# Kernel tuning notes

Measured on AMD Instinct MI355X. Metric: run time of the kernel, lower is better.

Reference implementation:

```python
import jax, jax.numpy as jnp
import numpy as np

STRIDE = 1
PAD = 1
DIL = 1


def setup_inputs() -> dict:
    key = jax.random.key(0)
    k1, k2, k3 = jax.random.split(key, 3)
    N, Cin, H, W = 8, 128, 96, 96
    Cout, Kh, Kw = 256, 3, 3
    inp = jax.random.normal(k1, (N, Cin, H, W), dtype=jnp.float32)
    # offset channels: 2*Kh*Kw per offset group (1 group), layout (dy, dx) pairs
    offset = jax.random.normal(k2, (N, 2 * Kh * Kw, H, W), dtype=jnp.float32)
    weight = jax.random.normal(k3, (Cout, Cin, Kh, Kw), dtype=jnp.float32) * 0.05
    return {"input": inp, "offset": offset, "weight": weight}


def _deform_conv(inp, offset, weight):
    N, Cin, H, W = inp.shape
    Cout, _, Kh, Kw = weight.shape
    K = Kh * Kw
    Ho = (H + 2 * PAD - DIL * (Kh - 1) - 1) // STRIDE + 1
    Wo = (W + 2 * PAD - DIL * (Kw - 1) - 1) // STRIDE + 1

    # base sampling grid (before learned offsets)
    hs = jnp.arange(Ho, dtype=inp.dtype) * STRIDE - PAD          # [Ho]
    ws = jnp.arange(Wo, dtype=inp.dtype) * STRIDE - PAD          # [Wo]
    ky, kx = jnp.meshgrid(jnp.arange(Kh, dtype=inp.dtype) * DIL,
                          jnp.arange(Kw, dtype=inp.dtype) * DIL,
                          indexing="ij")
    ky = ky.reshape(K)
    kx = kx.reshape(K)

    off = offset.reshape(N, K, 2, Ho, Wo)                        # pairs (dy, dx)
    py = hs[None, None, :, None] + ky[None, :, None, None] + off[:, :, 0]  # [N,K,Ho,Wo]
    px = ws[None, None, None, :] + kx[None, :, None, None] + off[:, :, 1]  # [N,K,Ho,Wo]

    y0 = jnp.floor(py)
    x0 = jnp.floor(px)
    ly = py - y0   # fractional parts
    lx = px - x0
    y0i = y0.astype(jnp.int32)
    x0i = x0.astype(jnp.int32)

    img = inp.transpose(0, 2, 3, 1)                              # [N,H,W,Cin]
    bidx = jnp.arange(N)[:, None, None, None]

    def gather(yi, xi):
        valid = (yi >= 0) & (yi < H) & (xi >= 0) & (xi < W)
        yc = jnp.clip(yi, 0, H - 1)
        xc = jnp.clip(xi, 0, W - 1)
        v = img[bidx, yc, xc]                                    # [N,K,Ho,Wo,Cin]
        return v * valid[..., None].astype(img.dtype)

    v00 = gather(y0i, x0i)
    v01 = gather(y0i, x0i + 1)
    v10 = gather(y0i + 1, x0i)
    v11 = gather(y0i + 1, x0i + 1)

    wy, wx = ly[..., None], lx[..., None]
    samp = (v00 * (1 - wy) * (1 - wx) + v01 * (1 - wy) * wx
            + v10 * wy * (1 - wx) + v11 * wy * wx)               # [N,K,Ho,Wo,Cin]

    w2 = weight.reshape(Cout, Cin, K)
    return jnp.einsum("nkhwc,ock->nohw", samp, w2)               # [N,Cout,Ho,Wo]


def reference(input, offset, weight):
    return _deform_conv(input, offset, weight)
```

## Files before the change

### kernel.cpp

```cpp
#include <hip/hip_runtime.h>
#include <hip/hip_bf16.h>
#include <hip/hip_fp16.h>

#define NN   8
#define CIN  128
#define HH   96
#define WW   96
#define COUT 256
#define KK   9
#define HO   96
#define WO   96
#define PTOT (NN*HO*WO)
#define BM   64
#define KTOT (CIN*KK)
#define KSTEPS (KTOT/32)

typedef _Float16 f16x8 __attribute__((ext_vector_type(8)));
typedef float f32x4  __attribute__((ext_vector_type(4)));

__device__ __forceinline__ __half2 u2h2(unsigned u) {
    union { unsigned u; __half2 h; } c; c.u = u; return c.h;
}
__device__ __forceinline__ unsigned h22u(__half2 h) {
    union { unsigned u; __half2 h; } c; c.h = h; return c.u;
}
__device__ __forceinline__ unsigned pack_h2(float a, float b) {
    auto v = __builtin_amdgcn_cvt_pkrtz(a, b);
    union { decltype(v) h; unsigned u; } c; c.h = v; return c.u;
}

__global__ __launch_bounds__(256) void to_nhwc_f16(const float* __restrict__ in,
                                                   unsigned short* __restrict__ outp) {
    __shared__ float tile[CIN * 97];
    const int ny = blockIdx.x;
    const int n = ny / HH, y = ny - n * HH;
    const float* src = in + (size_t)n * CIN * HH * WW + (size_t)y * WW;
    for (int i = threadIdx.x; i < CIN * WW; i += 256) {
        int c = i / WW, x = i - c * WW;
        tile[c * 97 + x] = src[(size_t)c * HH * WW + x];
    }
    __syncthreads();
    unsigned* dst = (unsigned*)(outp + (size_t)ny * WW * CIN);
    for (int i = threadIdx.x; i < (WW * CIN) / 2; i += 256) {
        int c2 = (i & 63) * 2;
        int x  = i >> 6;
        dst[x * (CIN / 2) + (c2 >> 1)] = pack_h2(tile[c2 * 97 + x], tile[(c2 + 1) * 97 + x]);
    }
}

__global__ __launch_bounds__(256) void w_pack(const float* __restrict__ w,
                                              unsigned short* __restrict__ wp) {
    int idx = blockIdx.x * 256 + threadIdx.x;
    if (idx >= KSTEPS * 16 * 64 * 8) return;
    int j  = idx & 7;
    int l  = (idx >> 3) & 63;
    int cb = (idx >> 9) & 15;
    int ks = idx >> 13;
    int co  = cb * 16 + (l & 15);
    int kg  = ks * 32 + ((l >> 4) * 8) + j;
    int tap = kg >> 7;
    int cin = kg & 127;
    _Float16 h = (_Float16)w[((size_t)co * CIN + cin) * KK + tap];
    wp[idx] = *(unsigned short*)&h;
}

#define GEOM_BYTES 6912
#define LDS_BYTES  39680
#define BUF0 6912
#define BUF1 23296

__global__ __launch_bounds__(512, 6) void deform_mfma(
    const unsigned short* __restrict__ imgB,
    const float*          __restrict__ off,
    const unsigned short* __restrict__ wPack,
    float*                __restrict__ out)
{
    __shared__ __align__(16) char smem[LDS_BYTES];
    unsigned* gOff = (unsigned*)smem;
    unsigned* gW0  = (unsigned*)(smem + 2304);
    unsigned* gW1  = (unsigned*)(smem + 4608);

    const int t    = threadIdx.x;
    const int lane = t & 63;
    const int wv   = t >> 6;

    const int bid  = ((blockIdx.x & 7) * ((PTOT / BM) >> 3)) + (blockIdx.x >> 3);

    const int p0   = bid * BM;
    const int nb   = p0 / (HO * WO);
    const int p0rem = p0 - nb * (HO * WO);

    for (int i = t; i < KK * BM; i += 512) {
        int tap = i >> 6, m = i & 63;
        int plin = p0rem + m;
        int ho = plin / WO, wo = plin - ho * WO;
        int kh = tap / 3, kw = tap - kh * 3;
        const float* ob = off + ((size_t)nb * 2 * KK + 2 * tap) * (HO * WO) + plin;
        float py = (float)(ho - 1 + kh) + ob[0];
        float px = (float)(wo - 1 + kw) + ob[HO * WO];
        float y0f = floorf(py), x0f = floorf(px);
        float ly = py - y0f, lx = px - x0f;
        int y0 = (int)y0f, x0 = (int)x0f;

        bool vy0 = (unsigned)y0 < (unsigned)HH;
        bool vy1 = (unsigned)(y0 + 1) < (unsigned)HH;
        bool vx0 = (unsigned)x0 < (unsigned)WW;
        bool vx1 = (unsigned)(x0 + 1) < (unsigned)WW;
        int yc0 = min(max(y0, 0), HH - 1);
        int yc1 = min(max(y0 + 1, 0), HH - 1);
        int xc0 = min(max(x0, 0), WW - 1);
        int xc1 = min(max(x0 + 1, 0), WW - 1);

        float w11 = ly * lx;
        float w10 = ly - w11;
        float w01 = lx - w11;
        float w00 = 1.f - ly - lx + w11;
        w00 = (vy0 && vx0) ? w00 : 0.f;
        w01 = (vy0 && vx1) ? w01 : 0.f;
        w10 = (vy1 && vx0) ? w10 : 0.f;
        w11 = (vy1 && vx1) ? w11 : 0.f;

        unsigned byte00 = (unsigned)(yc0 * WW + xc0) * (CIN * 2);
        unsigned xs = (xc1 != xc0) ? 1u : 0u;
        unsigned ys = (yc1 != yc0) ? 1u : 0u;
        gOff[i] = byte00 | (xs << 22) | (ys << 23);
        gW0[i]  = pack_h2(w00, w01);
        gW1[i]  = pack_h2(w10, w11);
    }

    f32x4 acc[4][2];
#pragma unroll
    for (int mf = 0; mf < 4; ++mf)
#pragma unroll
        for (int nf = 0; nf < 2; ++nf) acc[mf][nf] = (f32x4)0.f;

    const char* imgN = (const char*)(imgB + (size_t)nb * (HH * WW) * CIN);

    auto gather = [&](int tap, char* bufw) {
#pragma unroll
        for (int it = 0; it < 2; ++it) {
            int item  = t + it * 512;
            int pos   = item >> 4;
            int chunk = item & 15;
            int gi    = tap * 64 + pos;

            unsigned ofl  = gOff[gi];
            unsigned w0pk = gW0[gi];
            unsigned w1pk = gW1[gi];

            unsigned a00 = (ofl & 0x3fffffu) + (unsigned)(chunk * 16);
            unsigned dx  = (ofl >> 14) & 0x100u;
            unsigned dy  = ((ofl >> 23) & 1u) * 24576u;

            uint4 r00 = *(const uint4*)(imgN + a00);
            uint4 r01 = *(const uint4*)(imgN + a00 + dx);
            uint4 r10 = *(const uint4*)(imgN + a00 + dy);
            uint4 r11 = *(const uint4*)(imgN + a00 + dy + dx);

            unsigned u00 = w0pk & 0xffffu;      u00 |= u00 << 16;
            unsigned u01 = w0pk >> 16;          u01 |= u01 << 16;
            unsigned u10 = w1pk & 0xffffu;      u10 |= u10 << 16;
            unsigned u11 = w1pk >> 16;          u11 |= u11 << 16;
            __half2 w00s = u2h2(u00), w01s = u2h2(u01);
            __half2 w10s = u2h2(u10), w11s = u2h2(u11);

            unsigned pk[4];
            __half2 s;
            s = __hmul2(u2h2(r11.x), w11s);
            s = __hfma2(u2h2(r10.x), w10s, s);
            s = __hfma2(u2h2(r01.x), w01s, s);
            s = __hfma2(u2h2(r00.x), w00s, s);
            pk[0] = h22u(s);
            s = __hmul2(u2h2(r11.y), w11s);
            s = __hfma2(u2h2(r10.y), w10s, s);
            s = __hfma2(u2h2(r01.y), w01s, s);
            s = __hfma2(u2h2(r00.y), w00s, s);
            pk[1] = h22u(s);
            s = __hmul2(u2h2(r11.z), w11s);
            s = __hfma2(u2h2(r10.z), w10s, s);
            s = __hfma2(u2h2(r01.z), w01s, s);
            s = __hfma2(u2h2(r00.z), w00s, s);
            pk[2] = h22u(s);
            s = __hmul2(u2h2(r11.w), w11s);
            s = __hfma2(u2h2(r10.w), w10s, s);
            s = __hfma2(u2h2(r01.w), w01s, s);
            s = __hfma2(u2h2(r00.w), w00s, s);
            pk[3] = h22u(s);

            int byte = pos * 256 + chunk * 16;
            byte ^= (pos & 15) << 4;
            *(uint4*)(bufw + byte) = make_uint4(pk[0], pk[1], pk[2], pk[3]);
        }
    };

    __syncthreads();
    gather(0, smem + BUF0);

    for (int tap = 0; tap < KK; ++tap) {
        __syncthreads();
        const char* bufr = smem + ((tap & 1) ? BUF1 : BUF0);

#pragma unroll
        for (int cs = 0; cs < 4; ++cs) {
            int ks = tap * 4 + cs;
            f16x8 a[4], b[2];
#pragma unroll
            for (int mf = 0; mf < 4; ++mf) {
                int row  = mf * 16 + (lane & 15);
                int byte = row * 256 + cs * 64 + ((lane >> 4) * 16);
                byte ^= (row & 15) << 4;
                a[mf] = *(const f16x8*)(bufr + byte);
            }
#pragma unroll
            for (int nf = 0; nf < 2; ++nf) {
                int tile = ks * 16 + (wv * 2 + nf);
                b[nf] = *(const f16x8*)(wPack + (size_t)tile * 512 + lane * 8);
            }
            __builtin_amdgcn_s_setprio(1);
#pragma unroll
            for (int mf = 0; mf < 4; ++mf)
#pragma unroll
                for (int nf = 0; nf < 2; ++nf)
                    acc[mf][nf] = __builtin_amdgcn_mfma_f32_16x16x32_f16(
                        a[mf], b[nf], acc[mf][nf], 0, 0, 0);
            __builtin_amdgcn_s_setprio(0);
        }

        if (tap + 1 < KK) gather(tap + 1, smem + ((tap & 1) ? BUF0 : BUF1));
    }

    __syncthreads();
    float* cT = (float*)smem + wv * (32 * 20);
    const int colbase = lane & 15;
    const int rowq    = lane >> 4;
    const int co2     = lane & 31;
    const int half    = lane >> 5;
    float* outbase = out + ((size_t)nb * COUT + wv * 32 + co2) * (HO * WO) + p0rem;
#pragma unroll
    for (int mf = 0; mf < 4; ++mf) {
#pragma unroll
        for (int nf = 0; nf < 2; ++nf) {
            int co = nf * 16 + colbase;
            *(f32x4*)&cT[co * 20 + rowq * 4] = acc[mf][nf];
        }
        asm volatile("s_waitcnt lgkmcnt(0)" ::: "memory");
        __builtin_amdgcn_sched_barrier(0);
        f32x4 v0 = *(f32x4*)&cT[co2 * 20 + half * 8];
        f32x4 v1 = *(f32x4*)&cT[co2 * 20 + half * 8 + 4];
        *(float4*)(outbase + mf * 16 + half * 8)     = *(float4*)&v0;
        *(float4*)(outbase + mf * 16 + half * 8 + 4) = *(float4*)&v1;
    }
}

__global__ __launch_bounds__(256) void deform_fallback(const float* __restrict__ img,
                                                       const float* __restrict__ off,
                                                       const float* __restrict__ wgt,
                                                       float* __restrict__ out) {
    __shared__ float samp[8][CIN];
    const int tid = threadIdx.x;
    const int p0  = blockIdx.x * 8;
    const int n   = p0 / (HO * WO);
    const int rem = p0 % (HO * WO);
    const int ho  = rem / WO;
    const int wo0 = rem % WO;
    float acc[8];
#pragma unroll
    for (int t = 0; t < 8; ++t) acc[t] = 0.f;
    for (int k = 0; k < KK; ++k) {
        __syncthreads();
        const int kh = k / 3, kw = k % 3;
#pragma unroll
        for (int it = 0; it < 4; ++it) {
            int idx = tid + it * 256;
            int t   = idx >> 7;
            int c   = idx & (CIN - 1);
            int wo  = wo0 + t;
            float dy = off[(((size_t)n * 2 * KK + 2 * k) * HO + ho) * WO + wo];
            float dx = off[(((size_t)n * 2 * KK + 2 * k + 1) * HO + ho) * WO + wo];
            float py = (float)(ho - 1 + kh) + dy;
            float px = (float)(wo - 1 + kw) + dx;
            float y0f = floorf(py), x0f = floorf(px);
            float ly = py - y0f, lx = px - x0f;
            int y0 = (int)y0f, x0 = (int)x0f;
            float v00 = 0.f, v01 = 0.f, v10 = 0.f, v11 = 0.f;
            const float* base = img + ((size_t)n * CIN + c) * HH * WW;
            if ((unsigned)y0 < (unsigned)HH) {
                const float* row = base + (size_t)y0 * WW;
                if ((unsigned)x0 < (unsigned)WW)       v00 = row[x0];
                if ((unsigned)(x0 + 1) < (unsigned)WW) v01 = row[x0 + 1];
            }
            if ((unsigned)(y0 + 1) < (unsigned)HH) {
                const float* row = base + (size_t)(y0 + 1) * WW;
                if ((unsigned)x0 < (unsigned)WW)       v10 = row[x0];
                if ((unsigned)(x0 + 1) < (unsigned)WW) v11 = row[x0 + 1];
            }
            float top = v00 + lx * (v01 - v00);
            float bot = v10 + lx * (v11 - v10);
            samp[t][c] = top + ly * (bot - top);
        }
        __syncthreads();
        const float* wk = wgt + (size_t)tid * CIN * KK + k;
        for (int c = 0; c < CIN; c += 4) {
            float w0 = wk[(c + 0) * KK], w1 = wk[(c + 1) * KK];
            float w2 = wk[(c + 2) * KK], w3 = wk[(c + 3) * KK];
#pragma unroll
            for (int t = 0; t < 8; ++t) {
                const float4 s = *(const float4*)&samp[t][c];
                acc[t] = fmaf(s.x, w0, acc[t]);
                acc[t] = fmaf(s.y, w1, acc[t]);
                acc[t] = fmaf(s.z, w2, acc[t]);
                acc[t] = fmaf(s.w, w3, acc[t]);
            }
        }
    }
#pragma unroll
    for (int t = 0; t < 8; ++t)
        out[(((size_t)n * COUT + tid) * HO + ho) * WO + wo0 + t] = acc[t];
}

extern "C" void kernel_launch(void* const* d_in, const int* in_sizes, int n_in,
                              void* d_out, int out_size, void* d_ws, size_t ws_size,
                              hipStream_t stream) {
    const float* inp = (const float*)d_in[0];
    const float* off = (const float*)d_in[1];
    const float* wgt = (const float*)d_in[2];
    float* out = (float*)d_out;

    const size_t img_bytes = (size_t)NN * HH * WW * CIN * 2;
    const size_t wp_bytes  = (size_t)KSTEPS * 16 * 64 * 8 * 2;

    if (ws_size >= img_bytes + wp_bytes) {
        unsigned short* imgB  = (unsigned short*)d_ws;
        unsigned short* wPack = (unsigned short*)((char*)d_ws + img_bytes);
        to_nhwc_f16<<<NN * HH, 256, 0, stream>>>(inp, imgB);
        w_pack<<<(KSTEPS * 16 * 64 * 8) / 256, 256, 0, stream>>>(wgt, wPack);
        deform_mfma<<<PTOT / BM, 512, 0, stream>>>(imgB, off, wPack, out);
    } else {
        deform_fallback<<<PTOT / 8, 256, 0, stream>>>(inp, off, wgt, out);
    }
}
```

Before: 95.32 us.

## Precompute bilinear sampling geometry in a separate kernel and drop LDS staging

Moves the per-tap sampling geometry (clamped base address, edge flags, packed fp16 bilinear weights) out of the main MFMA kernel into a new geom_pack pre-pass that writes 16-byte records to workspace. The main kernel now reads these records from global memory on demand inside each gather, instead of computing them into LDS up front. This removes the prologue compute and a barrier and shrinks LDS from about 39.7 KB to 32 KB, which may allow more resident blocks. In exchange it adds an extra kernel launch and a global round trip of roughly 10 MB of geometry data.

Result: slower. 107.4 us (+12.7%).

```diff
diff --git a/kernel.cpp b/kernel.cpp
--- a/kernel.cpp
+++ b/kernel.cpp
@@ -10,6 +10,7 @@
 #define KK   9
 #define HO   96
 #define WO   96
+#define NPOS (HO*WO)
 #define PTOT (NN*HO*WO)
 #define BM   64
 #define KTOT (CIN*KK)
@@ -64,21 +65,59 @@
     wp[idx] = *(unsigned short*)&h;
 }
 
-#define GEOM_BYTES 6912
-#define LDS_BYTES  39680
-#define BUF0 6912
-#define BUF1 23296
+__global__ __launch_bounds__(256) void geom_pack(const float* __restrict__ off,
+                                                 uint4* __restrict__ gws) {
+    int idx = blockIdx.x * 256 + threadIdx.x;
+    if (idx >= NN * KK * NPOS) return;
+    int plin = idx % NPOS;
+    int r    = idx / NPOS;
+    int tap  = r % KK;
+    int n    = r / KK;
+    int ho = plin / WO, wo = plin - ho * WO;
+    int kh = tap / 3, kw = tap - kh * 3;
+    const float* ob = off + ((size_t)n * 2 * KK + 2 * tap) * NPOS + plin;
+    float py = (float)(ho - 1 + kh) + ob[0];
+    float px = (float)(wo - 1 + kw) + ob[NPOS];
+    float y0f = floorf(py), x0f = floorf(px);
+    float ly = py - y0f, lx = px - x0f;
+    int y0 = (int)y0f, x0 = (int)x0f;
+
+    bool vy0 = (unsigned)y0 < (unsigned)HH;
+    bool vy1 = (unsigned)(y0 + 1) < (unsigned)HH;
+    bool vx0 = (unsigned)x0 < (unsigned)WW;
+    bool vx1 = (unsigned)(x0 + 1) < (unsigned)WW;
+    int yc0 = min(max(y0, 0), HH - 1);
+    int yc1 = min(max(y0 + 1, 0), HH - 1);
+    int xc0 = min(max(x0, 0), WW - 1);
+    int xc1 = min(max(x0 + 1, 0), WW - 1);
+
+    float w11 = ly * lx;
+    float w10 = ly - w11;
+    float w01 = lx - w11;
+    float w00 = 1.f - ly - lx + w11;
+    w00 = (vy0 && vx0) ? w00 : 0.f;
+    w01 = (vy0 && vx1) ? w01 : 0.f;
+    w10 = (vy1 && vx0) ? w10 : 0.f;
+    w11 = (vy1 && vx1) ? w11 : 0.f;
+
+    unsigned byte00 = (unsigned)(yc0 * WW + xc0) * (CIN * 2);
+    unsigned xs = (xc1 != xc0) ? 1u : 0u;
+    unsigned ys = (yc1 != yc0) ? 1u : 0u;
+    gws[idx] = make_uint4(byte00 | (xs << 22) | (ys << 23),
+                          pack_h2(w00, w01), pack_h2(w10, w11), 0u);
+}
+
+#define LDS_BYTES  32768
+#define BUF0 0
+#define BUF1 16384
 
 __global__ __launch_bounds__(512, 6) void deform_mfma(
     const unsigned short* __restrict__ imgB,
-    const float*          __restrict__ off,
+    const uint4*          __restrict__ geomW,
     const unsigned short* __restrict__ wPack,
     float*                __restrict__ out)
 {
     __shared__ __align__(16) char smem[LDS_BYTES];
-    unsigned* gOff = (unsigned*)smem;
-    unsigned* gW0  = (unsigned*)(smem + 2304);
-    unsigned* gW1  = (unsigned*)(smem + 4608);
 
     const int t    = threadIdx.x;
     const int lane = t & 63;
@@ -87,46 +126,8 @@
     const int bid  = ((blockIdx.x & 7) * ((PTOT / BM) >> 3)) + (blockIdx.x >> 3);
 
     const int p0   = bid * BM;
-    const int nb   = p0 / (HO * WO);
-    const int p0rem = p0 - nb * (HO * WO);
-
-    for (int i = t; i < KK * BM; i += 512) {
-        int tap = i >> 6, m = i & 63;
-        int plin = p0rem + m;
-        int ho = plin / WO, wo = plin - ho * WO;
-        int kh = tap / 3, kw = tap - kh * 3;
-        const float* ob = off + ((size_t)nb * 2 * KK + 2 * tap) * (HO * WO) + plin;
-        float py = (float)(ho - 1 + kh) + ob[0];
-        float px = (float)(wo - 1 + kw) + ob[HO * WO];
-        float y0f = floorf(py), x0f = floorf(px);
-        float ly = py - y0f, lx = px - x0f;
-        int y0 = (int)y0f, x0 = (int)x0f;
-
-        bool vy0 = (unsigned)y0 < (unsigned)HH;
-        bool vy1 = (unsigned)(y0 + 1) < (unsigned)HH;
-        bool vx0 = (unsigned)x0 < (unsigned)WW;
-        bool vx1 = (unsigned)(x0 + 1) < (unsigned)WW;
-        int yc0 = min(max(y0, 0), HH - 1);
-        int yc1 = min(max(y0 + 1, 0), HH - 1);
-        int xc0 = min(max(x0, 0), WW - 1);
-        int xc1 = min(max(x0 + 1, 0), WW - 1);
-
-        float w11 = ly * lx;
-        float w10 = ly - w11;
-        float w01 = lx - w11;
-        float w00 = 1.f - ly - lx + w11;
-        w00 = (vy0 && vx0) ? w00 : 0.f;
-        w01 = (vy0 && vx1) ? w01 : 0.f;
-        w10 = (vy1 && vx0) ? w10 : 0.f;
-        w11 = (vy1 && vx1) ? w11 : 0.f;
-
-        unsigned byte00 = (unsigned)(yc0 * WW + xc0) * (CIN * 2);
-        unsigned xs = (xc1 != xc0) ? 1u : 0u;
-        unsigned ys = (yc1 != yc0) ? 1u : 0u;
-        gOff[i] = byte00 | (xs << 22) | (ys << 23);
-        gW0[i]  = pack_h2(w00, w01);
-        gW1[i]  = pack_h2(w10, w11);
-    }
+    const int nb   = p0 / NPOS;
+    const int p0rem = p0 - nb * NPOS;
 
     f32x4 acc[4][2];
 #pragma unroll
@@ -137,16 +138,17 @@
     const char* imgN = (const char*)(imgB + (size_t)nb * (HH * WW) * CIN);
 
     auto gather = [&](int tap, char* bufw) {
+        const uint4* gp = geomW + (size_t)(nb * KK + tap) * NPOS + p0rem;
 #pragma unroll
         for (int it = 0; it < 2; ++it) {
             int item  = t + it * 512;
             int pos   = item >> 4;
             int chunk = item & 15;
-            int gi    = tap * 64 + pos;
-
-            unsigned ofl  = gOff[gi];
-            unsigned w0pk = gW0[gi];
-            unsigned w1pk = gW1[gi];
+
+            uint4 g = gp[pos];
+            unsigned ofl  = g.x;
+            unsigned w0pk = g.y;
+            unsigned w1pk = g.z;
 
             unsigned a00 = (ofl & 0x3fffffu) + (unsigned)(chunk * 16);
             unsigned dx  = (ofl >> 14) & 0x100u;
@@ -193,7 +195,6 @@
         }
     };
 
-    __syncthreads();
     gather(0, smem + BUF0);
 
     for (int tap = 0; tap < KK; ++tap) {
@@ -326,15 +327,18 @@
     const float* wgt = (const float*)d_in[2];
     float* out = (float*)d_out;
 
-    const size_t img_bytes = (size_t)NN * HH * WW * CIN * 2;
-    const size_t wp_bytes  = (size_t)KSTEPS * 16 * 64 * 8 * 2;
-
-    if (ws_size >= img_bytes + wp_bytes) {
+    const size_t img_bytes  = (size_t)NN * HH * WW * CIN * 2;
+    const size_t wp_bytes   = (size_t)KSTEPS * 16 * 64 * 8 * 2;
+    const size_t geom_bytes = (size_t)NN * KK * NPOS * 16;
+
+    if (ws_size >= img_bytes + wp_bytes + geom_bytes) {
         unsigned short* imgB  = (unsigned short*)d_ws;
         unsigned short* wPack = (unsigned short*)((char*)d_ws + img_bytes);
+        uint4*          geomW = (uint4*)((char*)d_ws + img_bytes + wp_bytes);
         to_nhwc_f16<<<NN * HH, 256, 0, stream>>>(inp, imgB);
         w_pack<<<(KSTEPS * 16 * 64 * 8) / 256, 256, 0, stream>>>(wgt, wPack);
-        deform_mfma<<<PTOT / BM, 512, 0, stream>>>(imgB, off, wPack, out);
+        geom_pack<<<(NN * KK * NPOS + 255) / 256, 256, 0, stream>>>(off, geomW);
+        deform_mfma<<<PTOT / BM, 512, 0, stream>>>(imgB, geomW, wPack, out);
     } else {
         deform_fallback<<<PTOT / 8, 256, 0, stream>>>(inp, off, wgt, out);
     }
```

## Warp-specialize deform conv into producer gather waves and consumer MFMA waves

Applied to the files above, without the earlier changes.

Splits the 8 waves of each block into 4 producer waves, which do the bilinear gather into double-buffered LDS, and 4 consumer waves, which run the MFMAs over 64 output channels each. Producers issue all 16 global loads before doing any blending, for more memory-level parallelism. The goal is to overlap gather latency with matrix work instead of running the two in sequence in every wave. The cost is more registers per consumer wave (16 accumulator tiles), so the occupancy hint drops from 6 to 4, and only half the waves now do each job.

Result: slower. 102.4 us (+7.4%).

```diff
diff --git a/kernel.cpp b/kernel.cpp
--- a/kernel.cpp
+++ b/kernel.cpp
@@ -69,7 +69,7 @@
 #define BUF0 6912
 #define BUF1 23296
 
-__global__ __launch_bounds__(512, 6) void deform_mfma(
+__global__ __launch_bounds__(512, 4) void deform_mfma(
     const unsigned short* __restrict__ imgB,
     const float*          __restrict__ off,
     const unsigned short* __restrict__ wPack,
@@ -128,127 +128,134 @@
         gW1[i]  = pack_h2(w10, w11);
     }
 
-    f32x4 acc[4][2];
-#pragma unroll
-    for (int mf = 0; mf < 4; ++mf)
-#pragma unroll
-        for (int nf = 0; nf < 2; ++nf) acc[mf][nf] = (f32x4)0.f;
-
     const char* imgN = (const char*)(imgB + (size_t)nb * (HH * WW) * CIN);
 
-    auto gather = [&](int tap, char* bufw) {
-#pragma unroll
-        for (int it = 0; it < 2; ++it) {
-            int item  = t + it * 512;
-            int pos   = item >> 4;
-            int chunk = item & 15;
-            int gi    = tap * 64 + pos;
-
-            unsigned ofl  = gOff[gi];
-            unsigned w0pk = gW0[gi];
-            unsigned w1pk = gW1[gi];
-
-            unsigned a00 = (ofl & 0x3fffffu) + (unsigned)(chunk * 16);
-            unsigned dx  = (ofl >> 14) & 0x100u;
-            unsigned dy  = ((ofl >> 23) & 1u) * 24576u;
-
-            uint4 r00 = *(const uint4*)(imgN + a00);
-            uint4 r01 = *(const uint4*)(imgN + a00 + dx);
-            uint4 r10 = *(const uint4*)(imgN + a00 + dy);
-            uint4 r11 = *(const uint4*)(imgN + a00 + dy + dx);
-
-            unsigned u00 = w0pk & 0xffffu;      u00 |= u00 << 16;
-            unsigned u01 = w0pk >> 16;          u01 |= u01 << 16;
-            unsigned u10 = w1pk & 0xffffu;      u10 |= u10 << 16;
-            unsigned u11 = w1pk >> 16;          u11 |= u11 << 16;
-            __half2 w00s = u2h2(u00), w01s = u2h2(u01);
-            __half2 w10s = u2h2(u10), w11s = u2h2(u11);
-
-            unsigned pk[4];
-            __half2 s;
-            s = __hmul2(u2h2(r11.x), w11s);
-            s = __hfma2(u2h2(r10.x), w10s, s);
-            s = __hfma2(u2h2(r01.x), w01s, s);
-            s = __hfma2(u2h2(r00.x), w00s, s);
-            pk[0] = h22u(s);
-            s = __hmul2(u2h2(r11.y), w11s);
-            s = __hfma2(u2h2(r10.y), w10s, s);
-            s = __hfma2(u2h2(r01.y), w01s, s);
-            s = __hfma2(u2h2(r00.y), w00s, s);
-            pk[1] = h22u(s);
-            s = __hmul2(u2h2(r11.z), w11s);
-            s = __hfma2(u2h2(r10.z), w10s, s);
-            s = __hfma2(u2h2(r01.z), w01s, s);
-            s = __hfma2(u2h2(r00.z), w00s, s);
-            pk[2] = h22u(s);
-            s = __hmul2(u2h2(r11.w), w11s);
-            s = __hfma2(u2h2(r10.w), w10s, s);
-            s = __hfma2(u2h2(r01.w), w01s, s);
-            s = __hfma2(u2h2(r00.w), w00s, s);
-            pk[3] = h22u(s);
-
-            int byte = pos * 256 + chunk * 16;
-            byte ^= (pos & 15) << 4;
-            *(uint4*)(bufw + byte) = make_uint4(pk[0], pk[1], pk[2], pk[3]);
-        }
-    };
-
     __syncthreads();
-    gather(0, smem + BUF0);
-
-    for (int tap = 0; tap < KK; ++tap) {
+
+    if (wv < 4) {
+        auto gather = [&](int tap, char* bufw) {
+            uint4 r[4][4];
+            unsigned w0p[4], w1p[4];
+            int byt[4];
+#pragma unroll
+            for (int it = 0; it < 4; ++it) {
+                int item  = t + it * 256;
+                int pos   = item >> 4;
+                int chunk = item & 15;
+                int gi    = tap * 64 + pos;
+                unsigned ofl = gOff[gi];
+                w0p[it] = gW0[gi];
+                w1p[it] = gW1[gi];
+                unsigned a00 = (ofl & 0x3fffffu) + (unsigned)(chunk * 16);
+                unsigned dx  = (ofl >> 14) & 0x100u;
+                unsigned dy  = ((ofl >> 23) & 1u) * 24576u;
+                r[it][0] = *(const uint4*)(imgN + a00);
+                r[it][1] = *(const uint4*)(imgN + a00 + dx);
+                r[it][2] = *(const uint4*)(imgN + a00 + dy);
+                r[it][3] = *(const uint4*)(imgN + a00 + dy + dx);
+                int byte = pos * 256 + chunk * 16;
+                byt[it] = byte ^ ((pos & 15) << 4);
+            }
+#pragma unroll
+            for (int it = 0; it < 4; ++it) {
+                unsigned u00 = w0p[it] & 0xffffu;   u00 |= u00 << 16;
+                unsigned u01 = w0p[it] >> 16;       u01 |= u01 << 16;
+                unsigned u10 = w1p[it] & 0xffffu;   u10 |= u10 << 16;
+                unsigned u11 = w1p[it] >> 16;       u11 |= u11 << 16;
+                __half2 w00s = u2h2(u00), w01s = u2h2(u01);
+                __half2 w10s = u2h2(u10), w11s = u2h2(u11);
+
+                unsigned pk[4];
+                __half2 s;
+                s = __hmul2(u2h2(r[it][3].x), w11s);
+                s = __hfma2(u2h2(r[it][2].x), w10s, s);
+                s = __hfma2(u2h2(r[it][1].x), w01s, s);
+                s = __hfma2(u2h2(r[it][0].x), w00s, s);
+                pk[0] = h22u(s);
+                s = __hmul2(u2h2(r[it][3].y), w11s);
+                s = __hfma2(u2h2(r[it][2].y), w10s, s);
+                s = __hfma2(u2h2(r[it][1].y), w01s, s);
+                s = __hfma2(u2h2(r[it][0].y), w00s, s);
+                pk[1] = h22u(s);
+                s = __hmul2(u2h2(r[it][3].z), w11s);
+                s = __hfma2(u2h2(r[it][2].z), w10s, s);
+                s = __hfma2(u2h2(r[it][1].z), w01s, s);
+                s = __hfma2(u2h2(r[it][0].z), w00s, s);
+                pk[2] = h22u(s);
+                s = __hmul2(u2h2(r[it][3].w), w11s);
+                s = __hfma2(u2h2(r[it][2].w), w10s, s);
+                s = __hfma2(u2h2(r[it][1].w), w01s, s);
+                s = __hfma2(u2h2(r[it][0].w), w00s, s);
+                pk[3] = h22u(s);
+
+                *(uint4*)(bufw + byt[it]) = make_uint4(pk[0], pk[1], pk[2], pk[3]);
+            }
+        };
+
+        gather(0, smem + BUF0);
+        for (int tap = 0; tap < KK; ++tap) {
+            __syncthreads();
+            if (tap + 1 < KK) gather(tap + 1, smem + ((tap & 1) ? BUF0 : BUF1));
+        }
         __syncthreads();
-        const char* bufr = smem + ((tap & 1) ? BUF1 : BUF0);
-
-#pragma unroll
-        for (int cs = 0; cs < 4; ++cs) {
-            int ks = tap * 4 + cs;
-            f16x8 a[4], b[2];
-#pragma unroll
-            for (int mf = 0; mf < 4; ++mf) {
-                int row  = mf * 16 + (lane & 15);
-                int byte = row * 256 + cs * 64 + ((lane >> 4) * 16);
-                byte ^= (row & 15) << 4;
-                a[mf] = *(const f16x8*)(bufr + byte);
-            }
-#pragma unroll
-            for (int nf = 0; nf < 2; ++nf) {
-                int tile = ks * 16 + (wv * 2 + nf);
-                b[nf] = *(const f16x8*)(wPack + (size_t)tile * 512 + lane * 8);
-            }
-            __builtin_amdgcn_s_setprio(1);
-#pragma unroll
-            for (int mf = 0; mf < 4; ++mf)
-#pragma unroll
-                for (int nf = 0; nf < 2; ++nf)
-                    acc[mf][nf] = __builtin_amdgcn_mfma_f32_16x16x32_f16(
-                        a[mf], b[nf], acc[mf][nf], 0, 0, 0);
-            __builtin_amdgcn_s_setprio(0);
-        }
-
-        if (tap + 1 < KK) gather(tap + 1, smem + ((tap & 1) ? BUF0 : BUF1));
-    }
-
-    __syncthreads();
-    float* cT = (float*)smem + wv * (32 * 20);
-    const int colbase = lane & 15;
-    const int rowq    = lane >> 4;
-    const int co2     = lane & 31;
-    const int half    = lane >> 5;
-    float* outbase = out + ((size_t)nb * COUT + wv * 32 + co2) * (HO * WO) + p0rem;
-#pragma unroll
-    for (int mf = 0; mf < 4; ++mf) {
-#pragma unroll
-        for (int nf = 0; nf < 2; ++nf) {
-            int co = nf * 16 + colbase;
-            *(f32x4*)&cT[co * 20 + rowq * 4] = acc[mf][nf];
-        }
-        asm volatile("s_waitcnt lgkmcnt(0)" ::: "memory");
-        __builtin_amdgcn_sched_barrier(0);
-        f32x4 v0 = *(f32x4*)&cT[co2 * 20 + half * 8];
-        f32x4 v1 = *(f32x4*)&cT[co2 * 20 + half * 8 + 4];
-        *(float4*)(outbase + mf * 16 + half * 8)     = *(float4*)&v0;
-        *(float4*)(outbase + mf * 16 + half * 8 + 4) = *(float4*)&v1;
+    } else {
+        const int cw = wv - 4;
+        f32x4 acc[4][4];
+#pragma unroll
+        for (int mf = 0; mf < 4; ++mf)
+#pragma unroll
+            for (int nf = 0; nf < 4; ++nf) acc[mf][nf] = (f32x4)0.f;
+
+        for (int tap = 0; tap < KK; ++tap) {
+            __syncthreads();
+            const char* bufr = smem + ((tap & 1) ? BUF1 : BUF0);
+#pragma unroll
+            for (int cs = 0; cs < 4; ++cs) {
+                int ks = tap * 4 + cs;
+                f16x8 a[4], b[4];
+#pragma unroll
+                for (int mf = 0; mf < 4; ++mf) {
+                    int row  = mf * 16 + (lane & 15);
+                    int byte = row * 256 + cs * 64 + ((lane >> 4) * 16);
+                    byte ^= (row & 15) << 4;
+                    a[mf] = *(const f16x8*)(bufr + byte);
+                }
+#pragma unroll
+                for (int nf = 0; nf < 4; ++nf) {
+                    int tile = ks * 16 + (cw * 4 + nf);
+                    b[nf] = *(const f16x8*)(wPack + (size_t)tile * 512 + lane * 8);
+                }
+                __builtin_amdgcn_s_setprio(1);
+#pragma unroll
+                for (int mf = 0; mf < 4; ++mf)
+#pragma unroll
+                    for (int nf = 0; nf < 4; ++nf)
+                        acc[mf][nf] = __builtin_amdgcn_mfma_f32_16x16x32_f16(
+                            a[mf], b[nf], acc[mf][nf], 0, 0, 0);
+                __builtin_amdgcn_s_setprio(0);
+            }
+        }
+        __syncthreads();
+
+        float* cT = (float*)smem + cw * (64 * 20);
+        const int colbase = lane & 15;
+        const int rowq    = lane >> 4;
+        float* outbase = out + ((size_t)nb * COUT + cw * 64 + lane) * (HO * WO) + p0rem;
+#pragma unroll
+        for (int mf = 0; mf < 4; ++mf) {
+#pragma unroll
+            for (int nf = 0; nf < 4; ++nf) {
+                int co = nf * 16 + colbase;
+                *(f32x4*)&cT[co * 20 + rowq * 4] = acc[mf][nf];
+            }
+            asm volatile("s_waitcnt lgkmcnt(0)" ::: "memory");
+            __builtin_amdgcn_sched_barrier(0);
+#pragma unroll
+            for (int q = 0; q < 4; ++q) {
+                f32x4 v = *(f32x4*)&cT[lane * 20 + q * 4];
+                *(float4*)(outbase + mf * 16 + q * 4) = *(float4*)&v;
+            }
+        }
     }
 }
 
```

## Split fused deformable gather+GEMM into separate gather and GEMM kernels

Applied to the files above, without the earlier changes.

Splits the fused kernel in two. A gather kernel writes the bilinear-sampled f16 im2col matrix to workspace, and a GEMM kernel double-buffers tiles of that matrix through LDS into MFMA. The aim is to separate the latency-bound gather from the MFMA loop so each kernel can schedule better. The cost is a large global round trip of the sampled matrix (about 170 MB written then read) and one extra launch. The path is used only when the workspace is large enough; otherwise it falls back to the fused kernel.

After: 148.0 us. 1.55x slower.

```diff
diff --git a/kernel.cpp b/kernel.cpp
--- a/kernel.cpp
+++ b/kernel.cpp
@@ -64,30 +64,20 @@
     wp[idx] = *(unsigned short*)&h;
 }
 
-#define GEOM_BYTES 6912
-#define LDS_BYTES  39680
-#define BUF0 6912
-#define BUF1 23296
-
-__global__ __launch_bounds__(512, 6) void deform_mfma(
+__global__ __launch_bounds__(512, 6) void deform_gather(
     const unsigned short* __restrict__ imgB,
     const float*          __restrict__ off,
-    const unsigned short* __restrict__ wPack,
-    float*                __restrict__ out)
+    unsigned short*       __restrict__ samp)
 {
-    __shared__ __align__(16) char smem[LDS_BYTES];
+    __shared__ __align__(16) char smem[6912];
     unsigned* gOff = (unsigned*)smem;
     unsigned* gW0  = (unsigned*)(smem + 2304);
     unsigned* gW1  = (unsigned*)(smem + 4608);
 
-    const int t    = threadIdx.x;
-    const int lane = t & 63;
-    const int wv   = t >> 6;
-
-    const int bid  = ((blockIdx.x & 7) * ((PTOT / BM) >> 3)) + (blockIdx.x >> 3);
-
-    const int p0   = bid * BM;
-    const int nb   = p0 / (HO * WO);
+    const int t   = threadIdx.x;
+    const int bid = ((blockIdx.x & 7) * ((PTOT / BM) >> 3)) + (blockIdx.x >> 3);
+    const int p0  = bid * BM;
+    const int nb  = p0 / (HO * WO);
     const int p0rem = p0 - nb * (HO * WO);
 
     for (int i = t; i < KK * BM; i += 512) {
@@ -101,7 +91,6 @@
         float y0f = floorf(py), x0f = floorf(px);
         float ly = py - y0f, lx = px - x0f;
         int y0 = (int)y0f, x0 = (int)x0f;
-
         bool vy0 = (unsigned)y0 < (unsigned)HH;
         bool vy1 = (unsigned)(y0 + 1) < (unsigned)HH;
         bool vx0 = (unsigned)x0 < (unsigned)WW;
@@ -110,7 +99,6 @@
         int yc1 = min(max(y0 + 1, 0), HH - 1);
         int xc0 = min(max(x0, 0), WW - 1);
         int xc1 = min(max(x0 + 1, 0), WW - 1);
-
         float w11 = ly * lx;
         float w10 = ly - w11;
         float w01 = lx - w11;
@@ -119,7 +107,6 @@
         w01 = (vy0 && vx1) ? w01 : 0.f;
         w10 = (vy1 && vx0) ? w10 : 0.f;
         w11 = (vy1 && vx1) ? w11 : 0.f;
-
         unsigned byte00 = (unsigned)(yc0 * WW + xc0) * (CIN * 2);
         unsigned xs = (xc1 != xc0) ? 1u : 0u;
         unsigned ys = (yc1 != yc0) ? 1u : 0u;
@@ -127,16 +114,11 @@
         gW0[i]  = pack_h2(w00, w01);
         gW1[i]  = pack_h2(w10, w11);
     }
-
-    f32x4 acc[4][2];
-#pragma unroll
-    for (int mf = 0; mf < 4; ++mf)
-#pragma unroll
-        for (int nf = 0; nf < 2; ++nf) acc[mf][nf] = (f32x4)0.f;
+    __syncthreads();
 
     const char* imgN = (const char*)(imgB + (size_t)nb * (HH * WW) * CIN);
 
-    auto gather = [&](int tap, char* bufw) {
+    for (int tap = 0; tap < KK; ++tap) {
 #pragma unroll
         for (int it = 0; it < 2; ++it) {
             int item  = t + it * 512;
@@ -187,18 +169,53 @@
             s = __hfma2(u2h2(r00.w), w00s, s);
             pk[3] = h22u(s);
 
-            int byte = pos * 256 + chunk * 16;
-            byte ^= (pos & 15) << 4;
-            *(uint4*)(bufw + byte) = make_uint4(pk[0], pk[1], pk[2], pk[3]);
+            unsigned short* dst = samp + (size_t)(p0 + pos) * KTOT + tap * 128 + chunk * 8;
+            *(uint4*)dst = make_uint4(pk[0], pk[1], pk[2], pk[3]);
+        }
+    }
+}
+
+__global__ __launch_bounds__(512, 6) void deform_gemm(
+    const unsigned short* __restrict__ samp,
+    const unsigned short* __restrict__ wPack,
+    float*                __restrict__ out)
+{
+    __shared__ __align__(16) char smem[32768];
+
+    const int t    = threadIdx.x;
+    const int lane = t & 63;
+    const int wv   = t >> 6;
+
+    const int bid  = ((blockIdx.x & 7) * ((PTOT / BM) >> 3)) + (blockIdx.x >> 3);
+    const int p0   = bid * BM;
+    const int nb   = p0 / (HO * WO);
+    const int p0rem = p0 - nb * (HO * WO);
+
+    f32x4 acc[4][2];
+#pragma unroll
+    for (int mf = 0; mf < 4; ++mf)
+#pragma unroll
+        for (int nf = 0; nf < 2; ++nf) acc[mf][nf] = (f32x4)0.f;
+
+    const char* sampP = (const char*)samp;
+
+    auto stage = [&](int tap, char* bufw) {
+#pragma unroll
+        for (int j = 0; j < 2; ++j) {
+            int item = t + j * 512;
+            int row  = item >> 4;
+            int col  = (item & 15) * 16;
+            uint4 v = *(const uint4*)(sampP + (size_t)(p0 + row) * 2304 + tap * 256 + col);
+            int byte = row * 256 + (col ^ ((row & 15) << 4));
+            *(uint4*)(bufw + byte) = v;
         }
     };
 
-    __syncthreads();
-    gather(0, smem + BUF0);
+    stage(0, smem);
 
     for (int tap = 0; tap < KK; ++tap) {
         __syncthreads();
-        const char* bufr = smem + ((tap & 1) ? BUF1 : BUF0);
+        const char* bufr = smem + ((tap & 1) ? 16384 : 0);
 
 #pragma unroll
         for (int cs = 0; cs < 4; ++cs) {
@@ -226,6 +243,180 @@
             __builtin_amdgcn_s_setprio(0);
         }
 
+        if (tap + 1 < KK) stage(tap + 1, smem + ((tap & 1) ? 0 : 16384));
+    }
+
+    __syncthreads();
+    float* cT = (float*)smem + wv * (32 * 20);
+    const int colbase = lane & 15;
+    const int rowq    = lane >> 4;
+    const int co2     = lane & 31;
+    const int half    = lane >> 5;
+    float* outbase = out + ((size_t)nb * COUT + wv * 32 + co2) * (HO * WO) + p0rem;
+#pragma unroll
+    for (int mf = 0; mf < 4; ++mf) {
+#pragma unroll
+        for (int nf = 0; nf < 2; ++nf) {
+            int co = nf * 16 + colbase;
+            *(f32x4*)&cT[co * 20 + rowq * 4] = acc[mf][nf];
+        }
+        asm volatile("s_waitcnt lgkmcnt(0)" ::: "memory");
+        __builtin_amdgcn_sched_barrier(0);
+        f32x4 v0 = *(f32x4*)&cT[co2 * 20 + half * 8];
+        f32x4 v1 = *(f32x4*)&cT[co2 * 20 + half * 8 + 4];
+        *(float4*)(outbase + mf * 16 + half * 8)     = *(float4*)&v0;
+        *(float4*)(outbase + mf * 16 + half * 8 + 4) = *(float4*)&v1;
+    }
+}
+
+#define LDS_BYTES  39680
+#define BUF0 6912
+#define BUF1 23296
+
+__global__ __launch_bounds__(512, 6) void deform_mfma(
+    const unsigned short* __restrict__ imgB,
+    const float*          __restrict__ off,
+    const unsigned short* __restrict__ wPack,
+    float*                __restrict__ out)
+{
+    __shared__ __align__(16) char smem[LDS_BYTES];
+    unsigned* gOff = (unsigned*)smem;
+    unsigned* gW0  = (unsigned*)(smem + 2304);
+    unsigned* gW1  = (unsigned*)(smem + 4608);
+
+    const int t    = threadIdx.x;
+    const int lane = t & 63;
+    const int wv   = t >> 6;
+    const int bid  = ((blockIdx.x & 7) * ((PTOT / BM) >> 3)) + (blockIdx.x >> 3);
+    const int p0   = bid * BM;
+    const int nb   = p0 / (HO * WO);
+    const int p0rem = p0 - nb * (HO * WO);
+
+    for (int i = t; i < KK * BM; i += 512) {
+        int tap = i >> 6, m = i & 63;
+        int plin = p0rem + m;
+        int ho = plin / WO, wo = plin - ho * WO;
+        int kh = tap / 3, kw = tap - kh * 3;
+        const float* ob = off + ((size_t)nb * 2 * KK + 2 * tap) * (HO * WO) + plin;
+        float py = (float)(ho - 1 + kh) + ob[0];
+        float px = (float)(wo - 1 + kw) + ob[HO * WO];
+        float y0f = floorf(py), x0f = floorf(px);
+        float ly = py - y0f, lx = px - x0f;
+        int y0 = (int)y0f, x0 = (int)x0f;
+        bool vy0 = (unsigned)y0 < (unsigned)HH;
+        bool vy1 = (unsigned)(y0 + 1) < (unsigned)HH;
+        bool vx0 = (unsigned)x0 < (unsigned)WW;
+        bool vx1 = (unsigned)(x0 + 1) < (unsigned)WW;
+        int yc0 = min(max(y0, 0), HH - 1);
+        int yc1 = min(max(y0 + 1, 0), HH - 1);
+        int xc0 = min(max(x0, 0), WW - 1);
+        int xc1 = min(max(x0 + 1, 0), WW - 1);
+        float w11 = ly * lx;
+        float w10 = ly - w11;
+        float w01 = lx - w11;
+        float w00 = 1.f - ly - lx + w11;
+        w00 = (vy0 && vx0) ? w00 : 0.f;
+        w01 = (vy0 && vx1) ? w01 : 0.f;
+        w10 = (vy1 && vx0) ? w10 : 0.f;
+        w11 = (vy1 && vx1) ? w11 : 0.f;
+        unsigned byte00 = (unsigned)(yc0 * WW + xc0) * (CIN * 2);
+        unsigned xs = (xc1 != xc0) ? 1u : 0u;
+        unsigned ys = (yc1 != yc0) ? 1u : 0u;
+        gOff[i] = byte00 | (xs << 22) | (ys << 23);
+        gW0[i]  = pack_h2(w00, w01);
+        gW1[i]  = pack_h2(w10, w11);
+    }
+
+    f32x4 acc[4][2];
+#pragma unroll
+    for (int mf = 0; mf < 4; ++mf)
+#pragma unroll
+        for (int nf = 0; nf < 2; ++nf) acc[mf][nf] = (f32x4)0.f;
+
+    const char* imgN = (const char*)(imgB + (size_t)nb * (HH * WW) * CIN);
+
+    auto gather = [&](int tap, char* bufw) {
+#pragma unroll
+        for (int it = 0; it < 2; ++it) {
+            int item  = t + it * 512;
+            int pos   = item >> 4;
+            int chunk = item & 15;
+            int gi    = tap * 64 + pos;
+            unsigned ofl  = gOff[gi];
+            unsigned w0pk = gW0[gi];
+            unsigned w1pk = gW1[gi];
+            unsigned a00 = (ofl & 0x3fffffu) + (unsigned)(chunk * 16);
+            unsigned dx  = (ofl >> 14) & 0x100u;
+            unsigned dy  = ((ofl >> 23) & 1u) * 24576u;
+            uint4 r00 = *(const uint4*)(imgN + a00);
+            uint4 r01 = *(const uint4*)(imgN + a00 + dx);
+            uint4 r10 = *(const uint4*)(imgN + a00 + dy);
+            uint4 r11 = *(const uint4*)(imgN + a00 + dy + dx);
+            unsigned u00 = w0pk & 0xffffu;      u00 |= u00 << 16;
+            unsigned u01 = w0pk >> 16;          u01 |= u01 << 16;
+            unsigned u10 = w1pk & 0xffffu;      u10 |= u10 << 16;
+            unsigned u11 = w1pk >> 16;          u11 |= u11 << 16;
+            __half2 w00s = u2h2(u00), w01s = u2h2(u01);
+            __half2 w10s = u2h2(u10), w11s = u2h2(u11);
+            unsigned pk[4];
+            __half2 s;
+            s = __hmul2(u2h2(r11.x), w11s);
+            s = __hfma2(u2h2(r10.x), w10s, s);
+            s = __hfma2(u2h2(r01.x), w01s, s);
+            s = __hfma2(u2h2(r00.x), w00s, s);
+            pk[0] = h22u(s);
+            s = __hmul2(u2h2(r11.y), w11s);
+            s = __hfma2(u2h2(r10.y), w10s, s);
+            s = __hfma2(u2h2(r01.y), w01s, s);
+            s = __hfma2(u2h2(r00.y), w00s, s);
+            pk[1] = h22u(s);
+            s = __hmul2(u2h2(r11.z), w11s);
+            s = __hfma2(u2h2(r10.z), w10s, s);
+            s = __hfma2(u2h2(r01.z), w01s, s);
+            s = __hfma2(u2h2(r00.z), w00s, s);
+            pk[2] = h22u(s);
+            s = __hmul2(u2h2(r11.w), w11s);
+            s = __hfma2(u2h2(r10.w), w10s, s);
+            s = __hfma2(u2h2(r01.w), w01s, s);
+            s = __hfma2(u2h2(r00.w), w00s, s);
+            pk[3] = h22u(s);
+            int byte = pos * 256 + chunk * 16;
+            byte ^= (pos & 15) << 4;
+            *(uint4*)(bufw + byte) = make_uint4(pk[0], pk[1], pk[2], pk[3]);
+        }
+    };
+
+    __syncthreads();
+    gather(0, smem + BUF0);
+
+    for (int tap = 0; tap < KK; ++tap) {
+        __syncthreads();
+        const char* bufr = smem + ((tap & 1) ? BUF1 : BUF0);
+#pragma unroll
+        for (int cs = 0; cs < 4; ++cs) {
+            int ks = tap * 4 + cs;
+            f16x8 a[4], b[2];
+#pragma unroll
+            for (int mf = 0; mf < 4; ++mf) {
+                int row  = mf * 16 + (lane & 15);
+                int byte = row * 256 + cs * 64 + ((lane >> 4) * 16);
+                byte ^= (row & 15) << 4;
+                a[mf] = *(const f16x8*)(bufr + byte);
+            }
+#pragma unroll
+            for (int nf = 0; nf < 2; ++nf) {
+                int tile = ks * 16 + (wv * 2 + nf);
+                b[nf] = *(const f16x8*)(wPack + (size_t)tile * 512 + lane * 8);
+            }
+            __builtin_amdgcn_s_setprio(1);
+#pragma unroll
+            for (int mf = 0; mf < 4; ++mf)
+#pragma unroll
+                for (int nf = 0; nf < 2; ++nf)
+                    acc[mf][nf] = __builtin_amdgcn_mfma_f32_16x16x32_f16(
+                        a[mf], b[nf], acc[mf][nf], 0, 0, 0);
+            __builtin_amdgcn_s_setprio(0);
+        }
         if (tap + 1 < KK) gather(tap + 1, smem + ((tap & 1) ? BUF0 : BUF1));
     }
 
@@ -326,10 +517,19 @@
     const float* wgt = (const float*)d_in[2];
     float* out = (float*)d_out;
 
-    const size_t img_bytes = (size_t)NN * HH * WW * CIN * 2;
-    const size_t wp_bytes  = (size_t)KSTEPS * 16 * 64 * 8 * 2;
-
-    if (ws_size >= img_bytes + wp_bytes) {
+    const size_t img_bytes  = (size_t)NN * HH * WW * CIN * 2;
+    const size_t wp_bytes   = (size_t)KSTEPS * 16 * 64 * 8 * 2;
+    const size_t samp_bytes = (size_t)PTOT * KTOT * 2;
+
+    if (ws_size >= img_bytes + wp_bytes + samp_bytes) {
+        unsigned short* imgB  = (unsigned short*)d_ws;
+        unsigned short* wPack = (unsigned short*)((char*)d_ws + img_bytes);
+        unsigned short* samp  = (unsigned short*)((char*)d_ws + img_bytes + wp_bytes);
+        to_nhwc_f16<<<NN * HH, 256, 0, stream>>>(inp, imgB);
+        w_pack<<<(KSTEPS * 16 * 64 * 8) / 256, 256, 0, stream>>>(wgt, wPack);
+        deform_gather<<<PTOT / BM, 512, 0, stream>>>(imgB, off, samp);
+        deform_gemm<<<PTOT / BM, 512, 0, stream>>>(samp, wPack, out);
+    } else if (ws_size >= img_bytes + wp_bytes) {
         unsigned short* imgB  = (unsigned short*)d_ws;
         unsigned short* wPack = (unsigned short*)((char*)d_ws + img_bytes);
         to_nhwc_f16<<<NN * HH, 256, 0, stream>>>(inp, imgB);
```
